# Kernel tuning notes

Measured on AMD Instinct MI355X. Metric: run time of the kernel, lower is better.

The kernel has to match this reference:

```python
import jax, jax.numpy as jnp
import numpy as np

D = 1024


def setup_inputs() -> dict:
    key = jax.random.key(0)
    kx, kq, kk, kv, ko = jax.random.split(key, 5)
    scale = 0.02
    x = jax.random.normal(kx, (4, 2048, D), dtype=jnp.float32)
    Wq = jax.random.normal(kq, (D, D), dtype=jnp.float32) * scale
    Wk = jax.random.normal(kk, (D, D), dtype=jnp.float32) * scale
    Wv = jax.random.normal(kv, (D, D), dtype=jnp.float32) * scale
    Wo = jax.random.normal(ko, (D, D), dtype=jnp.float32) * scale
    return {"x": x, "Wq": Wq, "Wk": Wk, "Wv": Wv, "Wo": Wo}


def reference(x, Wq, Wk, Wv, Wo):
    # Linear projections (torch Linear: y = x @ W.T, no bias)
    q = jnp.einsum('bsd,ed->bse', x, Wq)
    k = jnp.einsum('bsd,ed->bse', x, Wk)
    v = jnp.einsum('bsd,ed->bse', x, Wv)
    d = x.shape[-1]
    # HRR binding: circular convolution of k and v along feature dim (rfft domain)
    Fk = jnp.fft.rfft(k, axis=-1)
    Fv = jnp.fft.rfft(v, axis=-1)
    Fq = jnp.fft.rfft(q, axis=-1)
    Fkv = Fk * Fv                      # bound key-value pairs, Fourier domain
    # causal cumulative memory over sequence; FFT is linear so cumsum commutes
    Fmem = jnp.cumsum(Fkv, axis=-2)    # [b, s, d//2+1] complex
    # unbind with query: circular correlation = multiply by conj(rfft(q))
    values_hat = jnp.fft.irfft(Fmem * jnp.conj(Fq), n=d, axis=-1)
    return jnp.einsum('bsd,ed->bse', values_hat, Wo)
```

## Files before the change

kernel.cpp:

```cpp
#include <hip/hip_runtime.h>

#define D_DIM 1024
#define NF 513
#define NB 4
#define NS 2048
#define NTOK (NB * NS)
#define NCH 32
#define CHS (NS / NCH)

typedef __attribute__((ext_vector_type(8))) short short8_t;
typedef __attribute__((ext_vector_type(4))) float f32x4;

__device__ inline unsigned short f2bf(float f) {
    unsigned u = __builtin_bit_cast(unsigned, f);
    u += 0x7FFFu + ((u >> 16) & 1u);
    return (unsigned short)(u >> 16);
}
__device__ inline float bf2f(unsigned short h) {
    unsigned u = ((unsigned)h) << 16;
    return __builtin_bit_cast(float, u);
}
__device__ inline unsigned pkc(float re, float im) {
    return (unsigned)f2bf(re) | ((unsigned)f2bf(im) << 16);
}
__device__ inline float2 upc(unsigned u) {
    return make_float2(bf2f((unsigned short)(u & 0xFFFFu)), bf2f((unsigned short)(u >> 16)));
}

__global__ __launch_bounds__(256) void convert_x(const float* __restrict__ src,
                                                 unsigned short* __restrict__ dst,
                                                 int n4) {
    int i = blockIdx.x * 256 + threadIdx.x;
    int stride = gridDim.x * 256;
    for (; i < n4; i += stride) {
        float4 v = reinterpret_cast<const float4*>(src)[i];
        ushort4 o;
        o.x = f2bf(v.x); o.y = f2bf(v.y); o.z = f2bf(v.z); o.w = f2bf(v.w);
        reinterpret_cast<ushort4*>(dst)[i] = o;
    }
}

__global__ __launch_bounds__(256) void convert_w(const float* __restrict__ Wq,
                                                 const float* __restrict__ Wk,
                                                 const float* __restrict__ Wv,
                                                 const float* __restrict__ Wo,
                                                 unsigned short* __restrict__ Wqkv,
                                                 unsigned short* __restrict__ Wob) {
    int y = blockIdx.y;
    const float* src = (y == 0) ? Wq : (y == 1) ? Wk : (y == 2) ? Wv : Wo;
    unsigned short* dst = (y < 3) ? (Wqkv + (size_t)y * 1048576) : Wob;
    int i = blockIdx.x * 256 + threadIdx.x;
    float4 v = reinterpret_cast<const float4*>(src)[i];
    ushort4 o;
    o.x = f2bf(v.x); o.y = f2bf(v.y); o.z = f2bf(v.z); o.w = f2bf(v.w);
    reinterpret_cast<ushort4*>(dst)[i] = o;
}

#define BM 128
#define BN 128
#define BK 32

__device__ inline void gload_lds16(const void* g, void* l) {
    __builtin_amdgcn_global_load_lds(
        (const __attribute__((address_space(1))) void*)g,
        (__attribute__((address_space(3))) void*)l,
        16, 0, 0);
}

template <typename OutT>
__global__ __launch_bounds__(256) void gemm_bf16_nt(const unsigned short* __restrict__ A,
                                                    const unsigned short* __restrict__ B,
                                                    OutT* __restrict__ C,
                                                    int M, int N, int K) {
    __shared__ __attribute__((aligned(16))) unsigned short ldsA[BM * BK];
    __shared__ __attribute__((aligned(16))) unsigned short ldsB[BN * BK];
    const int tid  = threadIdx.x;
    const int wave = tid >> 6;
    const int lane = tid & 63;
    const int l15  = lane & 15;
    const int k8   = (lane >> 4) << 3;
    const int wm   = (wave >> 1) * 64;
    const int wn   = (wave & 1) * 64;
    const int bm   = blockIdx.x * BM;
    const int bn   = blockIdx.y * BN;
    const int crow = tid >> 2;
    const int ccol = (tid & 3) << 3;

    f32x4 acc[4][4];
#pragma unroll
    for (int i = 0; i < 4; ++i)
#pragma unroll
        for (int j = 0; j < 4; ++j)
            acc[i][j] = (f32x4){0.f, 0.f, 0.f, 0.f};

    for (int k0 = 0; k0 < K; k0 += BK) {
        __syncthreads();
#pragma unroll
        for (int c = 0; c < 2; ++c) {
            int row = crow + (c << 6);
            gload_lds16(A + (size_t)(bm + row) * K + k0 + ccol, &ldsA[row * BK + ccol]);
            gload_lds16(B + (size_t)(bn + row) * K + k0 + ccol, &ldsB[row * BK + ccol]);
        }
        __syncthreads();

        short8_t af[4], bf[4];
#pragma unroll
        for (int mi = 0; mi < 4; ++mi)
            af[mi] = *reinterpret_cast<const short8_t*>(&ldsA[(wm + mi * 16 + l15) * BK + k8]);
#pragma unroll
        for (int ni = 0; ni < 4; ++ni)
            bf[ni] = *reinterpret_cast<const short8_t*>(&ldsB[(wn + ni * 16 + l15) * BK + k8]);
#pragma unroll
        for (int mi = 0; mi < 4; ++mi)
#pragma unroll
            for (int ni = 0; ni < 4; ++ni)
                acc[mi][ni] = __builtin_amdgcn_mfma_f32_16x16x32_bf16(af[mi], bf[ni], acc[mi][ni], 0, 0, 0);
    }

#pragma unroll
    for (int mi = 0; mi < 4; ++mi) {
        int rbase = bm + wm + mi * 16 + (lane >> 4) * 4;
#pragma unroll
        for (int ni = 0; ni < 4; ++ni) {
            int col = bn + wn + ni * 16 + l15;
#pragma unroll
            for (int j = 0; j < 4; ++j) {
                float v = acc[mi][ni][j];
                if constexpr (sizeof(OutT) == 4)
                    C[(size_t)(rbase + j) * N + col] = v;
                else
                    C[(size_t)(rbase + j) * N + col] = f2bf(v);
            }
        }
    }
}

__device__ inline int sw(int i) { return i ^ ((i >> 4) & 15); }

__device__ inline int dr4(int n) {
    return ((n & 3) << 8) | (((n >> 2) & 3) << 6) | (((n >> 4) & 3) << 4) |
           (((n >> 6) & 3) << 2) | ((n >> 8) & 3);
}

__device__ inline float2 cmul(float2 a, float2 b) {
    return make_float2(a.x * b.x - a.y * b.y, a.x * b.y + a.y * b.x);
}

__device__ inline void fft1024_r4(float2* X, const float2* tw, int t) {
#pragma unroll
    for (int s = 0; s < 5; ++s) {
        const int L = 1 << (2 * s);
        const int r = t & (L - 1);
        const int base = ((t >> (2 * s)) << (2 * s + 2)) + r;
        float2 A  = X[sw(base)];
        float2 Bv = X[sw(base + L)];
        float2 Cv = X[sw(base + 2 * L)];
        float2 Dv = X[sw(base + 3 * L)];
        if (s != 0) {
            const int step = 1024 >> (2 * s + 2);
            Bv = cmul(Bv, tw[sw(r * step)]);
            Cv = cmul(Cv, tw[sw(2 * r * step)]);
            Dv = cmul(Dv, tw[sw(3 * r * step)]);
        }
        float2 e0 = make_float2(A.x + Cv.x, A.y + Cv.y);
        float2 e1 = make_float2(A.x - Cv.x, A.y - Cv.y);
        float2 o0 = make_float2(Bv.x + Dv.x, Bv.y + Dv.y);
        float2 o1 = make_float2(Bv.x - Dv.x, Bv.y - Dv.y);
        X[sw(base)]         = make_float2(e0.x + o0.x, e0.y + o0.y);
        X[sw(base + L)]     = make_float2(e1.x + o1.y, e1.y - o1.x);
        X[sw(base + 2 * L)] = make_float2(e0.x - o0.x, e0.y - o0.y);
        X[sw(base + 3 * L)] = make_float2(e1.x - o1.y, e1.y + o1.x);
        __syncthreads();
    }
}

__global__ __launch_bounds__(256) void twiddle_init(float2* __restrict__ twg) {
    int k = blockIdx.x * 256 + threadIdx.x;
    if (k < 768) {
        float ang = -6.283185307179586f * (float)k / 1024.0f;
        float s, c;
        sincosf(ang, &s, &c);
        twg[sw(k)] = make_float2(c, s);
    }
}

__global__ __launch_bounds__(256) void hrr_fft_fwd(const unsigned short* __restrict__ QKV,
                                                   const float2* __restrict__ twg,
                                                   unsigned* __restrict__ Fkv,
                                                   unsigned* __restrict__ Fq) {
    __shared__ __attribute__((aligned(16))) float2 X[1024];
    __shared__ __attribute__((aligned(16))) float2 twL[768];
    const int tid = threadIdx.x;
    const int t0 = blockIdx.x * 2, t1 = t0 + 1;
    for (int i = tid; i < 384; i += 256)
        reinterpret_cast<float4*>(twL)[i] = reinterpret_cast<const float4*>(twg)[i];

#pragma unroll
    for (int which = 0; which < 2; ++which) {
        const int tok = which ? t1 : t0;
        const ushort4* Kr = (const ushort4*)(QKV + (size_t)tok * 3072 + 1024);
        const ushort4* Vr = (const ushort4*)(QKV + (size_t)tok * 3072 + 2048);
        ushort4 k4 = Kr[tid], v4 = Vr[tid];
        X[sw(dr4(4 * tid + 0))] = make_float2(bf2f(k4.x), bf2f(v4.x));
        X[sw(dr4(4 * tid + 1))] = make_float2(bf2f(k4.y), bf2f(v4.y));
        X[sw(dr4(4 * tid + 2))] = make_float2(bf2f(k4.z), bf2f(v4.z));
        X[sw(dr4(4 * tid + 3))] = make_float2(bf2f(k4.w), bf2f(v4.w));
        __syncthreads();
        fft1024_r4(X, twL, tid);
        for (int j = tid; j < NF; j += 256) {
            float2 Zj = X[sw(j)];
            float2 Zm = X[sw((1024 - j) & 1023)];
            float2 Fk = make_float2(0.5f * (Zj.x + Zm.x), 0.5f * (Zj.y - Zm.y));
            float2 Fv = make_float2(0.5f * (Zj.y + Zm.y), 0.5f * (Zm.x - Zj.x));
            float2 p = cmul(Fk, Fv);
            Fkv[(size_t)tok * NF + j] = pkc(p.x, p.y);
        }
        __syncthreads();
    }
    {
        const ushort4* Q0 = (const ushort4*)(QKV + (size_t)t0 * 3072);
        const ushort4* Q1 = (const ushort4*)(QKV + (size_t)t1 * 3072);
        ushort4 a4 = Q0[tid], b4 = Q1[tid];
        X[sw(dr4(4 * tid + 0))] = make_float2(bf2f(a4.x), bf2f(b4.x));
        X[sw(dr4(4 * tid + 1))] = make_float2(bf2f(a4.y), bf2f(b4.y));
        X[sw(dr4(4 * tid + 2))] = make_float2(bf2f(a4.z), bf2f(b4.z));
        X[sw(dr4(4 * tid + 3))] = make_float2(bf2f(a4.w), bf2f(b4.w));
        __syncthreads();
        fft1024_r4(X, twL, tid);
        for (int j = tid; j < NF; j += 256) {
            float2 Zj = X[sw(j)];
            float2 Zm = X[sw((1024 - j) & 1023)];
            Fq[(size_t)t0 * NF + j] = pkc(0.5f * (Zj.x + Zm.x), 0.5f * (Zj.y - Zm.y));
            Fq[(size_t)t1 * NF + j] = pkc(0.5f * (Zj.y + Zm.y), 0.5f * (Zm.x - Zj.x));
        }
    }
}

__global__ __launch_bounds__(256) void hrr_chunk_sum(const unsigned* __restrict__ Fkv,
                                                     float2* __restrict__ part) {
    int f = blockIdx.x * 256 + threadIdx.x;
    if (f >= NF) return;
    int ch = blockIdx.y, b = blockIdx.z;
    float sx = 0.f, sy = 0.f;
    size_t base = ((size_t)b * NS + (size_t)ch * CHS) * NF + f;
    for (int i = 0; i < CHS; ++i) {
        float2 t = upc(Fkv[base + (size_t)i * NF]);
        sx += t.x; sy += t.y;
    }
    part[(size_t)(b * NCH + ch) * NF + f] = make_float2(sx, sy);
}

__global__ __launch_bounds__(256) void hrr_scan_apply(unsigned* __restrict__ Fkv,
                                                      const unsigned* __restrict__ Fq,
                                                      const float2* __restrict__ part) {
    int f = blockIdx.x * 256 + threadIdx.x;
    if (f >= NF) return;
    int ch = blockIdx.y, b = blockIdx.z;
    float rx = 0.f, ry = 0.f;
    for (int c2 = 0; c2 < ch; ++c2) {
        float2 p = part[(size_t)(b * NCH + c2) * NF + f];
        rx += p.x; ry += p.y;
    }
    size_t base = ((size_t)b * NS + (size_t)ch * CHS) * NF + f;
    for (int i = 0; i < CHS; ++i) {
        size_t idx = base + (size_t)i * NF;
        float2 kv = upc(Fkv[idx]);
        rx += kv.x; ry += kv.y;
        float2 q = upc(Fq[idx]);
        Fkv[idx] = pkc(rx * q.x + ry * q.y, ry * q.x - rx * q.y);
    }
}

__global__ __launch_bounds__(256) void hrr_ifft(const unsigned* __restrict__ U,
                                                const float2* __restrict__ twg,
                                                unsigned short* __restrict__ vhat) {
    __shared__ __attribute__((aligned(16))) float2 X[1024];
    __shared__ __attribute__((aligned(16))) float2 twL[768];
    const int tid = threadIdx.x;
    const int t0 = blockIdx.x * 2, t1 = t0 + 1;
    for (int i = tid; i < 384; i += 256)
        reinterpret_cast<float4*>(twL)[i] = reinterpret_cast<const float4*>(twg)[i];
    const unsigned* U1 = U + (size_t)t0 * NF;
    const unsigned* U2 = U + (size_t)t1 * NF;
#pragma unroll
    for (int c = 0; c < 4; ++c) {
        int j = tid + (c << 8);
        float2 Cv;
        if (j <= 512) {
            float2 u1 = upc(U1[j]), u2 = upc(U2[j]);
            Cv = make_float2(u1.x - u2.y, -u1.y - u2.x);
        } else {
            int m = 1024 - j;
            float2 u1 = upc(U1[m]), u2 = upc(U2[m]);
            Cv = make_float2(u1.x + u2.y, u1.y - u2.x);
        }
        X[sw(dr4(j))] = Cv;
    }
    __syncthreads();
    fft1024_r4(X, twL, tid);
    const float invN = 1.0f / 1024.0f;
#pragma unroll
    for (int c = 0; c < 4; ++c) {
        int n = tid + (c << 8);
        float2 w = X[sw(n)];
        vhat[(size_t)t0 * D_DIM + n] = f2bf(w.x * invN);
        vhat[(size_t)t1 * D_DIM + n] = f2bf(-w.y * invN);
    }
}

extern "C" void kernel_launch(void* const* d_in, const int* in_sizes, int n_in,
                              void* d_out, int out_size, void* d_ws, size_t ws_size,
                              hipStream_t stream) {
    const float* x  = (const float*)d_in[0];
    const float* Wq = (const float*)d_in[1];
    const float* Wk = (const float*)d_in[2];
    const float* Wv = (const float*)d_in[3];
    const float* Wo = (const float*)d_in[4];
    float* out = (float*)d_out;

    char* ws = (char*)d_ws;
    unsigned short* QKVb = (unsigned short*)(ws + 0);
    unsigned*       Fkv  = (unsigned*)      (ws + 50331648);
    unsigned*       Fq   = (unsigned*)      (ws + 67141632);
    float2*         part = (float2*)        (ws + 83951616);
    float2*         twg  = (float2*)        (ws + 84476928);
    unsigned short* Wob  = (unsigned short*)(ws + 84483072);
    unsigned short* Wqkv = (unsigned short*)(ws + 86580224);
    unsigned short* xb   = (unsigned short*)(ws + 92871680);
    unsigned short* vhat = (unsigned short*)(ws + 109648896);

    convert_x<<<2048, 256, 0, stream>>>(x, xb, NTOK * D_DIM / 4);
    convert_w<<<dim3(1024, 4), 256, 0, stream>>>(Wq, Wk, Wv, Wo, Wqkv, Wob);
    twiddle_init<<<3, 256, 0, stream>>>(twg);

    dim3 gq(NTOK / BM, 3072 / BN);
    gemm_bf16_nt<unsigned short><<<gq, 256, 0, stream>>>(xb, Wqkv, QKVb, NTOK, 3072, D_DIM);

    hrr_fft_fwd<<<NTOK / 2, 256, 0, stream>>>(QKVb, twg, Fkv, Fq);

    dim3 gs((NF + 255) / 256, NCH, NB);
    hrr_chunk_sum<<<gs, 256, 0, stream>>>(Fkv, part);
    hrr_scan_apply<<<gs, 256, 0, stream>>>(Fkv, Fq, part);

    hrr_ifft<<<NTOK / 2, 256, 0, stream>>>(Fkv, twg, vhat);

    dim3 go(NTOK / BM, D_DIM / BN);
    gemm_bf16_nt<float><<<go, 256, 0, stream>>>(vhat, Wob, out, NTOK, D_DIM, D_DIM);
}
```

Baseline: 184.2 us.

## Triple-buffer GEMM LDS tiles with async global-to-LDS prefetch pipeline

Replaces the single-buffer load/sync/compute loop in the bf16 GEMM with a three-stage LDS ring. Tiles are prefetched two iterations ahead, and explicit vmcnt waits and barriers replace the double __syncthreads per step. MFMA issue is wrapped in s_setprio to favour compute waves. This is meant to hide global load latency behind the matrix math, at the cost of triple the LDS footprint, which may reduce occupancy.

Result: faster. 175.6 us (-4.7%).

```diff
diff --git a/kernel.cpp b/kernel.cpp
--- a/kernel.cpp
+++ b/kernel.cpp
@@ -72,8 +72,8 @@
                                                     const unsigned short* __restrict__ B,
                                                     OutT* __restrict__ C,
                                                     int M, int N, int K) {
-    __shared__ __attribute__((aligned(16))) unsigned short ldsA[BM * BK];
-    __shared__ __attribute__((aligned(16))) unsigned short ldsB[BN * BK];
+    __shared__ __attribute__((aligned(16))) unsigned short ldsA[3 * BM * BK];
+    __shared__ __attribute__((aligned(16))) unsigned short ldsB[3 * BN * BK];
     const int tid  = threadIdx.x;
     const int wave = tid >> 6;
     const int lane = tid & 63;
@@ -85,6 +85,11 @@
     const int bn   = blockIdx.y * BN;
     const int crow = tid >> 2;
     const int ccol = (tid & 3) << 3;
+    const int NT   = K / BK;
+
+    const unsigned short* Arow = A + (size_t)(bm + crow) * K + ccol;
+    const unsigned short* Brow = B + (size_t)(bn + crow) * K + ccol;
+    const size_t rstep = (size_t)64 * K;
 
     f32x4 acc[4][4];
 #pragma unroll
@@ -93,28 +98,49 @@
         for (int j = 0; j < 4; ++j)
             acc[i][j] = (f32x4){0.f, 0.f, 0.f, 0.f};
 
-    for (int k0 = 0; k0 < K; k0 += BK) {
-        __syncthreads();
-#pragma unroll
-        for (int c = 0; c < 2; ++c) {
-            int row = crow + (c << 6);
-            gload_lds16(A + (size_t)(bm + row) * K + k0 + ccol, &ldsA[row * BK + ccol]);
-            gload_lds16(B + (size_t)(bn + row) * K + k0 + ccol, &ldsB[row * BK + ccol]);
-        }
-        __syncthreads();
-
-        short8_t af[4], bf[4];
+    auto STAGE = [&](int t, int b) {
+        const int k0 = t * BK;
+        unsigned short* la = &ldsA[b * (BM * BK) + crow * BK + ccol];
+        unsigned short* lb = &ldsB[b * (BM * BK) + crow * BK + ccol];
+        gload_lds16(Arow + k0, la);
+        gload_lds16(Brow + k0, lb);
+        gload_lds16(Arow + rstep + k0, la + 64 * BK);
+        gload_lds16(Brow + rstep + k0, lb + 64 * BK);
+    };
+
+    STAGE(0, 0);
+    STAGE(1, 1);
+
+    for (int j = 0; j < NT; ++j) {
+        const int buf = j % 3;
+        if (j + 2 < NT) STAGE(j + 2, (j + 2) % 3);
+
+        if (j + 2 < NT)      asm volatile("s_waitcnt vmcnt(8)" ::: "memory");
+        else if (j + 1 < NT) asm volatile("s_waitcnt vmcnt(4)" ::: "memory");
+        else                 asm volatile("s_waitcnt vmcnt(0)" ::: "memory");
+        __builtin_amdgcn_s_barrier();
+        asm volatile("" ::: "memory");
+
+        const unsigned short* la = &ldsA[buf * (BM * BK)];
+        const unsigned short* lb = &ldsB[buf * (BM * BK)];
+        short8_t af[4], bfv[4];
 #pragma unroll
         for (int mi = 0; mi < 4; ++mi)
-            af[mi] = *reinterpret_cast<const short8_t*>(&ldsA[(wm + mi * 16 + l15) * BK + k8]);
+            af[mi] = *reinterpret_cast<const short8_t*>(&la[(wm + mi * 16 + l15) * BK + k8]);
 #pragma unroll
         for (int ni = 0; ni < 4; ++ni)
-            bf[ni] = *reinterpret_cast<const short8_t*>(&ldsB[(wn + ni * 16 + l15) * BK + k8]);
+            bfv[ni] = *reinterpret_cast<const short8_t*>(&lb[(wn + ni * 16 + l15) * BK + k8]);
+
+        __builtin_amdgcn_s_setprio(1);
 #pragma unroll
         for (int mi = 0; mi < 4; ++mi)
 #pragma unroll
             for (int ni = 0; ni < 4; ++ni)
-                acc[mi][ni] = __builtin_amdgcn_mfma_f32_16x16x32_bf16(af[mi], bf[ni], acc[mi][ni], 0, 0, 0);
+                acc[mi][ni] = __builtin_amdgcn_mfma_f32_16x16x32_bf16(af[mi], bfv[ni], acc[mi][ni], 0, 0, 0);
+        __builtin_amdgcn_s_setprio(0);
+
+        __builtin_amdgcn_s_barrier();
+        asm volatile("" ::: "memory");
     }
 
 #pragma unroll
```
